# Performance work log

Measured on AMD Instinct MI355X. Metric: run time of the kernel, lower is better.

Reference implementation:

```python
import jax, jax.numpy as jnp
import numpy as np

VAR0, VAR1 = 0.1, 0.2   # cfg['variance']
THRESH = 0.5            # overlap_thresh
THETA = 0.01
NEGPOS = 3


def decode(loc, priors):
    # priors center-form [P,4]; returns point-form boxes [P,4]
    cxcy = priors[:, :2] + loc[:, :2] * VAR0 * priors[:, 2:]
    wh = priors[:, 2:] * jnp.exp(loc[:, 2:] * VAR1)
    return jnp.concatenate([cxcy - wh * 0.5, cxcy + wh * 0.5], axis=1)


def center_size(b):
    return jnp.concatenate([(b[:, :2] + b[:, 2:]) * 0.5, b[:, 2:] - b[:, :2]], axis=1)


def encode(matched, priors_c):
    # matched point-form [P,4], priors_c center-form [P,4]
    g_cxcy = ((matched[:, :2] + matched[:, 2:]) * 0.5 - priors_c[:, :2]) / (VAR0 * priors_c[:, 2:])
    g_wh = jnp.log((matched[:, 2:] - matched[:, :2]) / priors_c[:, 2:]) / VAR1
    return jnp.concatenate([g_cxcy, g_wh], axis=1)


def jaccard(a, b):
    # a [G,4], b [P,4] point form -> IoU [G,P]
    lt = jnp.maximum(a[:, None, :2], b[None, :, :2])
    rb = jnp.minimum(a[:, None, 2:], b[None, :, 2:])
    wh = jnp.clip(rb - lt, 0.0)
    inter = wh[..., 0] * wh[..., 1]
    area_a = ((a[:, 2] - a[:, 0]) * (a[:, 3] - a[:, 1]))[:, None]
    area_b = ((b[:, 2] - b[:, 0]) * (b[:, 3] - b[:, 1]))[None, :]
    return inter / (area_a + area_b - inter)


def _match_one(truths, labels, gt_mask, arm_loc, priors):
    # refine_match with arm_loc (use_ARM=True path)
    P = priors.shape[0]
    G = truths.shape[0]
    dec = decode(arm_loc, priors)                                 # [P,4]
    ov = jnp.where(gt_mask[:, None], jaccard(truths, dec), -1.0)  # [G,P], padded GT masked out
    best_prior_idx = jnp.argmax(ov, axis=1)                       # [G]
    best_truth_ov = jnp.max(ov, axis=0)                           # [P]
    best_truth_idx = jnp.argmax(ov, axis=0)                       # [P]
    safe = jnp.where(gt_mask, best_prior_idx, P)                  # OOB index -> dropped scatter
    best_truth_ov = best_truth_ov.at[safe].set(2.0, mode='drop')  # force-match each valid GT
    best_truth_idx = best_truth_idx.at[safe].set(jnp.arange(G), mode='drop')
    matched = truths[best_truth_idx]                              # [P,4]
    conf = jnp.where(best_truth_ov < THRESH, 0, labels[best_truth_idx])
    loc = encode(matched, center_size(dec))
    return loc, conf


def forward(arm_loc, arm_conf, odm_loc, odm_conf, priors, targets, num_gts):
    B, P, C = odm_conf.shape
    truths = targets[..., :4]
    labels = targets[..., 4].astype(jnp.int32)
    gt_mask = jnp.arange(targets.shape[1])[None, :] < num_gts[:, None]
    loc_t, conf_t = jax.vmap(_match_one, in_axes=(0, 0, 0, 0, None))(
        truths, labels, gt_mask,
        jax.lax.stop_gradient(arm_loc), jax.lax.stop_gradient(priors))
    loc_t = jax.lax.stop_gradient(loc_t)    # loc_t.requires_grad = False
    conf_t = jax.lax.stop_gradient(conf_t)

    # ARM objectness filter on positives
    p_obj = jax.nn.softmax(arm_conf, axis=2)[:, :, 1]
    pos = (conf_t > 0) & (p_obj > THETA)

    # masked smooth-L1 localization loss (sum)
    posf = pos[..., None].astype(odm_loc.dtype)
    d = jnp.abs(odm_loc * posf - loc_t * posf)
    loss_l = jnp.sum(jnp.where(d < 1.0, 0.5 * d * d, d - 0.5))

    # hard negative mining on per-prior softmax loss
    batch_conf = odm_conf.reshape(-1, C)
    lc = jax.nn.logsumexp(batch_conf, axis=1) - jnp.take_along_axis(
        batch_conf, conf_t.reshape(-1, 1), axis=1)[:, 0]
    lc = jnp.where(pos.reshape(-1), 0.0, lc).reshape(B, P)
    loss_idx = jnp.argsort(-lc, axis=1)
    idx_rank = jnp.argsort(loss_idx, axis=1)
    num_pos = jnp.sum(pos.astype(jnp.int32), axis=1, keepdims=True)  # [B,1]
    num_neg = jnp.minimum(NEGPOS * num_pos, P - 1)
    neg = idx_rank < num_neg
    mask = pos | neg

    # masked cross entropy (compute on zeroed-out logits like the original, then mask)
    conf_p = (odm_conf * mask[..., None].astype(odm_conf.dtype)).reshape(-1, C)
    tgt = jnp.where(mask, conf_t, 0).reshape(-1)
    logp = jax.nn.log_softmax(conf_p, axis=1)
    ce = -jnp.take_along_axis(logp, tgt[:, None], axis=1)[:, 0]
    loss_c = jnp.sum(ce * mask.reshape(-1).astype(ce.dtype))

    N = jnp.sum(num_pos).astype(jnp.float32)
    return loss_l / N, loss_c / N


def setup_inputs():
    key = jax.random.key(0)
    ks = jax.random.split(key, 10)
    B, P, C, G = 32, 16320, 21, 40
    arm_loc = jax.random.normal(ks[0], (B, P, 4), jnp.float32) * 0.1
    arm_conf = jax.random.normal(ks[1], (B, P, 2), jnp.float32)
    odm_loc = jax.random.normal(ks[2], (B, P, 4), jnp.float32) * 0.1
    odm_conf = jax.random.normal(ks[3], (B, P, C), jnp.float32)
    # priors in center form with positive sizes
    pc = jax.random.uniform(ks[4], (P, 2), jnp.float32, 0.1, 0.9)
    pwh = jax.random.uniform(ks[5], (P, 2), jnp.float32, 0.05, 0.3)
    priors = jnp.concatenate([pc, pwh], axis=1)
    # GT boxes in point form with positive area, labels in 1..C-1, padded to G=40
    gc = jax.random.uniform(ks[6], (B, G, 2), jnp.float32, 0.2, 0.8)
    gwh = jax.random.uniform(ks[7], (B, G, 2), jnp.float32, 0.05, 0.3)
    boxes = jnp.concatenate([gc - gwh * 0.5, gc + gwh * 0.5], axis=-1)
    labels = jax.random.randint(ks[8], (B, G, 1), 1, C).astype(jnp.float32)
    targets = jnp.concatenate([boxes, labels], axis=-1)
    num_gts = jax.random.randint(ks[9], (B,), 1, G + 1).astype(jnp.int32)
    return {"arm_loc": arm_loc, "arm_conf": arm_conf, "odm_loc": odm_loc,
            "odm_conf": odm_conf, "priors": priors, "targets": targets,
            "num_gts": num_gts}


def reference(arm_loc, arm_conf, odm_loc, odm_conf, priors, targets, num_gts):
    return forward(arm_loc, arm_conf, odm_loc, odm_conf, priors, targets, num_gts)
```

## Files before the change

kernel.cpp:

```cpp
#include <hip/hip_runtime.h>
#include <math.h>

#define VAR0 0.1f
#define VAR1 0.2f
#define THRESH 0.5f
#define THETA 0.01f
#define MAXG 64
#define BLK 256
#define SELT 1024
#define NCH 16
#define NB 4096
#define CAP 2048
#define NST 6

__device__ __forceinline__ float fdiv_fast(float a, float b) { return __fdividef(a, b); }

__device__ __forceinline__ float4 decode_box(float4 l, float4 pr) {
    float cx = pr.x + l.x * VAR0 * pr.z;
    float cy = pr.y + l.y * VAR0 * pr.w;
    float w = pr.z * __expf(l.z * VAR1);
    float h = pr.w * __expf(l.w * VAR1);
    return make_float4(cx - w * 0.5f, cy - h * 0.5f, cx + w * 0.5f, cy + h * 0.5f);
}

__device__ __forceinline__ float smooth_l1_sum(float4 ol, float4 t, float4 d) {
    float pcx = (d.x + d.z) * 0.5f, pcy = (d.y + d.w) * 0.5f;
    float pw = d.z - d.x, ph = d.w - d.y;
    float g0 = fdiv_fast((t.x + t.z) * 0.5f - pcx, VAR0 * pw);
    float g1 = fdiv_fast((t.y + t.w) * 0.5f - pcy, VAR0 * ph);
    float g2 = __logf(fdiv_fast(t.z - t.x, pw)) * (1.0f / VAR1);
    float g3 = __logf(fdiv_fast(t.w - t.y, ph)) * (1.0f / VAR1);
    float s = 0.f, dd;
    dd = fabsf(ol.x - g0); s += (dd < 1.f) ? 0.5f*dd*dd : dd - 0.5f;
    dd = fabsf(ol.y - g1); s += (dd < 1.f) ? 0.5f*dd*dd : dd - 0.5f;
    dd = fabsf(ol.z - g2); s += (dd < 1.f) ? 0.5f*dd*dd : dd - 0.5f;
    dd = fabsf(ol.w - g3); s += (dd < 1.f) ? 0.5f*dd*dd : dd - 0.5f;
    return s;
}

__device__ __forceinline__ float softmax_pobj(float2 c) {
    float mm = fmaxf(c.x, c.y);
    float e0 = __expf(c.x - mm), e1 = __expf(c.y - mm);
    return fdiv_fast(e1, e0 + e1);
}

__device__ __forceinline__ float iou_ov(float4 t, float areaA, float4 d, float areaB) {
    float lt0 = fmaxf(t.x, d.x), lt1 = fmaxf(t.y, d.y);
    float rb0 = fminf(t.z, d.z), rb1 = fminf(t.w, d.w);
    float w = rb0 - lt0; if (w < 0.f) w = 0.f;
    float h = rb1 - lt1; if (h < 0.f) h = 0.f;
    float inter = w * h;
    return fdiv_fast(inter, areaA + areaB - inter);
}

__device__ __forceinline__ unsigned wave_umax_bits(unsigned v) {
    int x = (int)v;
    int t;
    t = __builtin_amdgcn_update_dpp(0, x, 0x111, 0xf, 0xf, true);  x = (t > x) ? t : x;
    t = __builtin_amdgcn_update_dpp(0, x, 0x112, 0xf, 0xf, true);  x = (t > x) ? t : x;
    t = __builtin_amdgcn_update_dpp(0, x, 0x114, 0xf, 0xf, true);  x = (t > x) ? t : x;
    t = __builtin_amdgcn_update_dpp(0, x, 0x118, 0xf, 0xf, true);  x = (t > x) ? t : x;
    t = __builtin_amdgcn_update_dpp(0, x, 0x142, 0xa, 0xf, false); x = (t > x) ? t : x;
    t = __builtin_amdgcn_update_dpp(0, x, 0x143, 0xc, 0xf, false); x = (t > x) ? t : x;
    return (unsigned)__builtin_amdgcn_readlane(x, 63);
}

__global__ __launch_bounds__(BLK) void k_main2(
        const float* __restrict__ arm_loc, const float* __restrict__ priors,
        const float* __restrict__ arm_conf, const float* __restrict__ odm_loc,
        const float* __restrict__ odm_conf,
        const float* __restrict__ targets, const int* __restrict__ num_gts,
        float* __restrict__ ce, unsigned char* __restrict__ posm,
        unsigned* __restrict__ bb, unsigned long long* __restrict__ bpw,
        float* __restrict__ partL, int* __restrict__ partN, int* __restrict__ counter,
        int B, int P, int C, int G) {
    int b = blockIdx.y;
    int p0 = blockIdx.x * BLK;
    int tid = threadIdx.x;
    int p = p0 + tid;
    int lane = tid & 63, wid = tid >> 6;
    int wavebase = p0 + (tid & ~63);
    __shared__ float4 st4[MAXG];
    __shared__ float  stl[MAXG];
    __shared__ float  sarea[MAXG];
    __shared__ unsigned long long wk[4][MAXG];
    __shared__ float oc_s[BLK * 21];
    __shared__ float rl[BLK];
    __shared__ int   rc[BLK];
    __shared__ int sng;
    if (blockIdx.x == 0 && blockIdx.y == 0 && tid == 0) *counter = 0;
    if (tid == 0) sng = num_gts[b];
    for (int g = tid; g < G; g += BLK) {
        const float* tg = targets + (size_t)b * G * 5 + g * 5;
        float t0 = tg[0], t1 = tg[1], t2 = tg[2], t3 = tg[3];
        st4[g] = make_float4(t0, t1, t2, t3);
        stl[g] = tg[4];
        sarea[g] = (t2 - t0) * (t3 - t1);
    }
    __syncthreads();

    int nrows = P - p0; if (nrows > BLK) nrows = BLK;
    int nf = nrows * C;
    int nf4 = nf >> 2;
    const float4* ocb4 = (const float4*)(odm_conf + ((size_t)b * P + p0) * C);
    float4 stg[NST];
    #pragma unroll
    for (int r = 0; r < NST; ++r) {
        int idx = r * BLK + tid;
        stg[r] = (idx < nf4) ? ocb4[idx] : make_float4(0.f, 0.f, 0.f, 0.f);
    }

    int ng = sng;
    bool ok = p < P;
    float4 d = make_float4(0.f, 0.f, 0.f, 0.f);
    float areaB = 0.f;
    size_t i = (size_t)b * P + (ok ? p : 0);
    if (ok) {
        float4 l = ((const float4*)arm_loc)[i];
        float4 pr = ((const float4*)priors)[p];
        d = decode_box(l, pr);
        areaB = (d.z - d.x) * (d.w - d.y);
    }
    float bov = -2.0f; int bidx = 0;
    int g = 0;
    for (; g + 2 <= ng; g += 2) {
        float4 t0g = st4[g], t1g = st4[g + 1];
        unsigned vb0 = 0u, vb1 = 0u;
        if (ok) {
            float ov0 = iou_ov(t0g, sarea[g], d, areaB);
            float ov1 = iou_ov(t1g, sarea[g + 1], d, areaB);
            if (ov0 > bov) { bov = ov0; bidx = g; }
            if (ov1 > bov) { bov = ov1; bidx = g + 1; }
            vb0 = __float_as_uint(ov0);
            vb1 = __float_as_uint(ov1);
        }
        unsigned om0 = wave_umax_bits(vb0);
        unsigned om1 = wave_umax_bits(vb1);
        unsigned long long m0 = __ballot(ok && vb0 == om0);
        unsigned long long m1 = __ballot(ok && vb1 == om1);
        if (lane == 0) {
            unsigned long long k0 = 0ull, k1 = 0ull;
            if (m0) {
                int pw = wavebase + (int)__builtin_ctzll(m0);
                k0 = ((unsigned long long)om0 << 32)
                   | (unsigned long long)(0xFFFFFFFFu - (unsigned)pw);
            }
            if (m1) {
                int pw = wavebase + (int)__builtin_ctzll(m1);
                k1 = ((unsigned long long)om1 << 32)
                   | (unsigned long long)(0xFFFFFFFFu - (unsigned)pw);
            }
            wk[wid][g] = k0;
            wk[wid][g + 1] = k1;
        }
    }
    if (g < ng) {
        float4 tg = st4[g];
        unsigned vb = 0u;
        if (ok) {
            float ov = iou_ov(tg, sarea[g], d, areaB);
            if (ov > bov) { bov = ov; bidx = g; }
            vb = __float_as_uint(ov);
        }
        unsigned om = wave_umax_bits(vb);
        unsigned long long m = __ballot(ok && vb == om);
        if (lane == 0) {
            unsigned long long k0 = 0ull;
            if (m) {
                int pw = wavebase + (int)__builtin_ctzll(m);
                k0 = ((unsigned long long)om << 32)
                   | (unsigned long long)(0xFFFFFFFFu - (unsigned)pw);
            }
            wk[wid][g] = k0;
        }
    }

    float lsum = 0.f; int pc = 0;
    int conf_t = 0;
    if (ok) {
        conf_t = (bov < THRESH) ? 0 : (int)stl[bidx];
        float p_obj = softmax_pobj(((const float2*)arm_conf)[i]);
        bool pos = (conf_t > 0) && (p_obj > THETA);
        if (pos) {
            pc = 1;
            float4 ol = ((const float4*)odm_loc)[i];
            lsum = smooth_l1_sum(ol, st4[bidx], d);
        }
        posm[i] = pos ? 1 : 0;
        bb[i] = (__float_as_uint(bov) & 0xFFFFFFC0u) | (unsigned)bidx;
    }
    rl[tid] = lsum; rc[tid] = pc;

    #pragma unroll
    for (int r = 0; r < NST; ++r) {
        int idx = r * BLK + tid;
        if (idx < nf4) ((float4*)oc_s)[idx] = stg[r];
    }
    for (int t = (nf4 << 2) + tid; t < nf; t += BLK) oc_s[t] = ((const float*)ocb4)[t];
    __syncthreads();

    if (tid < ng) {
        unsigned long long k0 = wk[0][tid], k1 = wk[1][tid];
        unsigned long long k2 = wk[2][tid], k3 = wk[3][tid];
        unsigned long long m01 = k0 > k1 ? k0 : k1;
        unsigned long long m23 = k2 > k3 ? k2 : k3;
        unsigned long long m = m01 > m23 ? m01 : m23;
        bpw[(size_t)(b * G + tid) * gridDim.x + blockIdx.x] = m;
    }

    if (ok) {
        const float* oc = oc_s + tid * C;
        float mx = oc[0];
        for (int j = 1; j < C; ++j) mx = fmaxf(mx, oc[j]);
        float sume = 0.f;
        for (int j = 0; j < C; ++j) sume += __expf(oc[j] - mx);
        float lse = mx + __logf(sume);
        ce[i] = lse - oc[conf_t];
    }

    for (int off = BLK / 2; off > 0; off >>= 1) {
        if (tid < off) { rl[tid] += rl[tid + off]; rc[tid] += rc[tid + off]; }
        __syncthreads();
    }
    if (tid == 0) {
        partL[b * gridDim.x + blockIdx.x] = rl[0];
        partN[b * gridDim.x + blockIdx.x] = rc[0];
    }
}

__global__ __launch_bounds__(SELT) void k_tail(
        const float* __restrict__ arm_loc, const float* __restrict__ priors,
        const float* __restrict__ arm_conf, const float* __restrict__ odm_loc,
        const float* __restrict__ odm_conf,
        const float* __restrict__ targets, const int* __restrict__ num_gts,
        const unsigned long long* __restrict__ bpw, const unsigned* __restrict__ bb,
        float* __restrict__ ce, unsigned char* __restrict__ posm,
        const float* __restrict__ partL, const int* __restrict__ partN,
        float* __restrict__ partC, float* __restrict__ totL, int* __restrict__ npos,
        int* __restrict__ counter, float* __restrict__ out,
        int NBX, int B, int P, int C, int G) {
    int b = blockIdx.x;
    int tid = threadIdx.x;
    int lane = tid & 63, wid = tid >> 6;
    __shared__ int fp[MAXG];
    __shared__ float4 st4[MAXG];
    __shared__ float  stl[MAXG];
    __shared__ float  pdl[MAXG];
    __shared__ int    pdn[MAXG];
    __shared__ unsigned hist[NB];
    __shared__ float cv[CAP];
    __shared__ int   ci[CAP];
    __shared__ int   sums[SELT];
    __shared__ int   redi[16];
    __shared__ float redf[16];
    __shared__ int sh_base[16];
    __shared__ int sh_m, sh_b1, sh_k1, sh_npos, sh_istar, sh_kk, sh_cum, sh_last;
    __shared__ unsigned sh_T, sh_pref;
    __shared__ float sh_mx, sh_totl;
    __shared__ int sng;
    if (tid == 0) sng = num_gts[b];
    for (int g = tid; g < G; g += SELT) {
        const float* tg = targets + (size_t)b * G * 5 + g * 5;
        st4[g] = make_float4(tg[0], tg[1], tg[2], tg[3]);
        stl[g] = tg[4];
        pdl[g] = 0.f; pdn[g] = 0;
    }
    __syncthreads();
    int ng = sng;

    for (int g = wid; g < ng; g += 16) {
        const unsigned long long* src = bpw + (size_t)(b * G + g) * NBX;
        unsigned long long key = 0ull;
        for (int j = lane; j < NBX; j += 64) {
            unsigned long long v = src[j];
            if (v > key) key = v;
        }
        for (int off = 32; off > 0; off >>= 1) {
            unsigned long long o = __shfl_down(key, (unsigned)off, 64);
            if (o > key) key = o;
        }
        if (lane == 0) fp[g] = (int)(0xFFFFFFFFu - (unsigned)(key & 0xFFFFFFFFull));
    }
    __syncthreads();

    if (tid < ng) {
        int g = tid;
        bool dup = false;
        for (int g2 = g + 1; g2 < ng; ++g2) if (fp[g2] == fp[g]) { dup = true; break; }
        if (!dup) {
            int p = fp[g];
            size_t i = (size_t)b * P + p;
            unsigned bbv = bb[i];
            int old_bidx = (int)(bbv & 63u);
            bool old_ge = __uint_as_float(bbv & 0xFFFFFFC0u) >= THRESH;
            int old_ct = old_ge ? (int)stl[old_bidx] : 0;
            int new_ct = (int)stl[g];
            float p_obj = softmax_pobj(((const float2*)arm_conf)[i]);
            bool old_pos = (old_ct > 0) && (p_obj > THETA);
            bool new_pos = (p_obj > THETA);
            float dL = 0.f;
            if (old_pos || new_pos) {
                float4 l = ((const float4*)arm_loc)[i];
                float4 pr = ((const float4*)priors)[p];
                float4 d = decode_box(l, pr);
                float4 ol = ((const float4*)odm_loc)[i];
                if (old_pos) dL -= smooth_l1_sum(ol, st4[old_bidx], d);
                if (new_pos) dL += smooth_l1_sum(ol, st4[g], d);
            }
            pdl[g] = dL;
            pdn[g] = (new_pos ? 1 : 0) - (old_pos ? 1 : 0);
            const float* oc = odm_conf + i * (size_t)C;
            float ce_old = ce[i];
            float ce_new = (old_ct == new_ct) ? ce_old
                         : (ce_old + oc[old_ct] - oc[new_ct]);
            ce[i] = ce_new;
            posm[i] = new_pos ? 1 : 0;
        }
    }
    __syncthreads();

    int c0 = 0; float l0 = 0.f;
    for (int j = tid; j < NBX; j += SELT) { c0 += partN[b * NBX + j]; l0 += partL[b * NBX + j]; }
    for (int g = tid; g < G; g += SELT)   { c0 += pdn[g];             l0 += pdl[g]; }
    for (int off = 32; off > 0; off >>= 1) {
        c0 += __shfl_down(c0, (unsigned)off, 64);
        l0 += __shfl_down(l0, (unsigned)off, 64);
    }
    if (lane == 0) { redi[wid] = c0; redf[wid] = l0; }
    __syncthreads();
    if (tid < 64) {
        int v = (tid < 16) ? redi[tid] : 0;
        float f = (tid < 16) ? redf[tid] : 0.f;
        for (int off = 32; off > 0; off >>= 1) {
            v += __shfl_down(v, (unsigned)off, 64);
            f += __shfl_down(f, (unsigned)off, 64);
        }
        if (tid == 0) { sh_npos = v; sh_totl = f; }
    }
    __syncthreads();
    int npos_b = sh_npos;
    long K = 3L * npos_b;
    if (K > P - 1) K = P - 1;

    unsigned cb[NCH];
    unsigned lv[NCH];
    unsigned pmw = 0u;
    const unsigned* ceb = (const unsigned*)ce + (size_t)b * P;
    const unsigned char* pb = posm + (size_t)b * P;
    #pragma unroll
    for (int c = 0; c < NCH; ++c) {
        int i = c * SELT + tid;
        unsigned cbits = (i < P) ? ceb[i] : 0u;
        bool ps = (i < P) && (pb[i] != 0);
        cb[c] = cbits;
        if (ps) pmw |= (1u << c);
        lv[c] = ps ? 0u : cbits;
    }

    unsigned uT = 0xFFFFFFFFu; int istar = -1;
    if (K > 0) {
        float mx = 0.f;
        #pragma unroll
        for (int c = 0; c < NCH; ++c) mx = fmaxf(mx, __uint_as_float(lv[c]));
        for (int off = 32; off > 0; off >>= 1) mx = fmaxf(mx, __shfl_xor(mx, off, 64));
        if (lane == 0) redf[wid] = mx;
        __syncthreads();
        if (tid == 0) {
            float v = redf[0];
            for (int w = 1; w < 16; ++w) v = fmaxf(v, redf[w]);
            sh_mx = v;
        }
        __syncthreads();
        float vmax = sh_mx;
        float scale = (vmax > 0.f) ? ((float)NB / vmax) : 0.f;

        for (int j = tid; j < NB; j += SELT) hist[j] = 0u;
        __syncthreads();
        #pragma unroll
        for (int c = 0; c < NCH; ++c) {
            int i = c * SELT + tid;
            if (i < P) {
                int bn = (int)(__uint_as_float(lv[c]) * scale);
                if (bn > NB - 1) bn = NB - 1;
                atomicAdd(&hist[bn], 1u);
            }
        }
        __syncthreads();

        int s4 = (int)(hist[4*tid] + hist[4*tid+1] + hist[4*tid+2] + hist[4*tid+3]);
        sums[SELT - 1 - tid] = s4;
        __syncthreads();
        int x = sums[tid];
        int xs = x;
        for (int off = 1; off < 64; off <<= 1) {
            int o = __shfl_up(xs, (unsigned)off, 64);
            if (lane >= off) xs += o;
        }
        if (lane == 63) redi[wid] = xs;
        __syncthreads();
        if (tid < 64) {
            int v = (tid < 16) ? redi[tid] : 0;
            int vs = v;
            for (int off = 1; off < 16; off <<= 1) {
                int o = __shfl_up(vs, (unsigned)off, 64);
                if (lane >= off) vs += o;
            }
            if (tid < 16) redi[tid] = vs - v;
        }
        __syncthreads();
        int excl_rev = xs + redi[wid] - x;
        sums[tid] = excl_rev;
        __syncthreads();
        int suf = sums[SELT - 1 - tid];
        {
            int run = suf;
            for (int j = 3; j >= 0; --j) {
                int bin = 4 * tid + j;
                int h = (int)hist[bin];
                if ((long)run < K && K <= (long)run + h) { sh_b1 = bin; sh_k1 = (int)(K - run); }
                run += h;
            }
        }
        __syncthreads();
        int B1 = sh_b1, k1 = sh_k1;

        if (tid == 0) sh_m = 0;
        __syncthreads();
        #pragma unroll
        for (int c = 0; c < NCH; ++c) {
            int i = c * SELT + tid;
            if (i < P) {
                float f = __uint_as_float(lv[c]);
                int bn = (int)(f * scale);
                if (bn > NB - 1) bn = NB - 1;
                if (bn == B1) {
                    int pos = atomicAdd(&sh_m, 1);
                    if (pos < CAP) { cv[pos] = f; ci[pos] = i; }
                }
            }
        }
        __syncthreads();
        int m = sh_m;
        if (m <= CAP) {
            for (int j = tid; j < m; j += SELT) {
                float vj = cv[j]; int ij = ci[j]; int r = 0;
                for (int jj = 0; jj < m; ++jj) {
                    float vx = cv[jj];
                    r += (vx > vj || (vx == vj && ci[jj] < ij)) ? 1 : 0;
                }
                if (r == k1 - 1) { sh_T = __float_as_uint(vj); sh_istar = ij; }
            }
            __syncthreads();
            uT = sh_T; istar = sh_istar;
        } else {
            if (tid == 0) { sh_pref = 0u; sh_kk = (int)K; }
            __syncthreads();
            for (int bit = 30; bit >= 0; --bit) {
                unsigned pref = sh_pref;
                int kk = sh_kk;
                unsigned hi = pref >> (bit + 1);
                int cnt = 0;
                #pragma unroll
                for (int c = 0; c < NCH; ++c) {
                    int i = c * SELT + tid;
                    unsigned v = lv[c];
                    cnt += ((i < P) && ((v >> (bit + 1)) == hi) && ((v >> bit) & 1u)) ? 1 : 0;
                }
                for (int off = 32; off > 0; off >>= 1) cnt += __shfl_down(cnt, (unsigned)off, 64);
                if (lane == 0) redi[wid] = cnt;
                __syncthreads();
                if (tid < 64) {
                    int v = (tid < 16) ? redi[tid] : 0;
                    for (int off = 32; off > 0; off >>= 1) v += __shfl_down(v, (unsigned)off, 64);
                    if (tid == 0) {
                        if (kk <= v) sh_pref = pref | (1u << bit);
                        else sh_kk = kk - v;
                    }
                }
                __syncthreads();
            }
            unsigned T = sh_pref; int krem = sh_kk;
            if (tid == 0) { sh_istar = -1; sh_cum = 0; }
            __syncthreads();
            for (int c = 0; c < NCH; ++c) {
                int i = c * SELT + tid;
                bool eq = (i < P) && (lv[c] == T);
                unsigned long long mk = __ballot(eq);
                if (lane == 0) redi[wid] = (int)__popcll(mk);
                __syncthreads();
                if (tid < 64) {
                    int v = (tid < 16) ? redi[tid] : 0;
                    for (int off = 1; off < 16; off <<= 1) {
                        int o = __shfl_up(v, (unsigned)off, 64);
                        if (lane >= off) v += o;
                    }
                    if (tid < 16) sh_base[tid] = v;
                }
                __syncthreads();
                int cum = sh_cum;
                int base = (wid == 0) ? 0 : sh_base[wid - 1];
                if (eq) {
                    int r = cum + base + (int)__popcll(mk & ((1ull << lane) - 1ull));
                    if (r == krem - 1) sh_istar = i;
                }
                __syncthreads();
                if (tid == 0) sh_cum = cum + sh_base[15];
                __syncthreads();
                if (sh_cum >= krem) break;
            }
            __syncthreads();
            uT = T; istar = sh_istar;
        }
    }

    float cs = 0.f;
    #pragma unroll
    for (int c = 0; c < NCH; ++c) {
        int i = c * SELT + tid;
        if (i < P) {
            unsigned v = lv[c];
            bool sel = ((pmw >> c) & 1u) || (v > uT) || (v == uT && i <= istar);
            if (sel) cs += __uint_as_float(cb[c]);
        }
    }
    for (int off = 32; off > 0; off >>= 1) cs += __shfl_down(cs, (unsigned)off, 64);
    if (lane == 0) redf[wid] = cs;
    __syncthreads();
    if (tid < 64) {
        float v = (tid < 16) ? redf[tid] : 0.f;
        for (int off = 32; off > 0; off >>= 1) v += __shfl_down(v, (unsigned)off, 64);
        if (tid == 0) {
            partC[b] = v; npos[b] = npos_b; totL[b] = sh_totl;
            __threadfence();
            int old = atomicAdd(counter, 1);
            sh_last = (old == B - 1) ? 1 : 0;
        }
    }
    __syncthreads();

    if (sh_last && tid < 64) {
        float aL = 0.f, aC = 0.f; int aN = 0;
        if (tid < B) {
            aL = atomicAdd(&totL[tid], 0.0f);
            aC = atomicAdd(&partC[tid], 0.0f);
            aN = atomicAdd(&npos[tid], 0);
        }
        for (int off = 32; off > 0; off >>= 1) {
            aL += __shfl_down(aL, (unsigned)off, 64);
            aC += __shfl_down(aC, (unsigned)off, 64);
            aN += __shfl_down(aN, (unsigned)off, 64);
        }
        if (tid == 0) {
            float N = (float)aN;
            out[0] = aL / N;
            out[1] = aC / N;
        }
    }
}

extern "C" void kernel_launch(void* const* d_in, const int* in_sizes, int n_in,
                              void* d_out, int out_size, void* d_ws, size_t ws_size,
                              hipStream_t stream) {
    const float* arm_loc  = (const float*)d_in[0];
    const float* arm_conf = (const float*)d_in[1];
    const float* odm_loc  = (const float*)d_in[2];
    const float* odm_conf = (const float*)d_in[3];
    const float* priors   = (const float*)d_in[4];
    const float* targets  = (const float*)d_in[5];
    const int*   num_gts  = (const int*)d_in[6];
    float* out = (float*)d_out;

    int B = in_sizes[6];
    int P = in_sizes[4] / 4;
    int C = in_sizes[3] / (B * P);
    int G = in_sizes[5] / (B * 5);
    int NBX = (P + BLK - 1) / BLK;

    char* ws = (char*)d_ws;
    size_t off = 0;
    auto alloc = [&](size_t bytes) -> void* {
        void* ptr = ws + off;
        off = (off + bytes + 255) & ~(size_t)255;
        return ptr;
    };
    unsigned long long* bpw = (unsigned long long*)alloc((size_t)B * G * NBX * 8);
    unsigned* bb = (unsigned*)alloc((size_t)B * P * 4);
    float* ce  = (float*)alloc((size_t)B * P * sizeof(float));
    unsigned char* posm = (unsigned char*)alloc((size_t)B * P);
    float* partL = (float*)alloc((size_t)B * NBX * sizeof(float));
    int* partN   = (int*)alloc((size_t)B * NBX * sizeof(int));
    float* partC = (float*)alloc((size_t)B * sizeof(float));
    float* totL  = (float*)alloc((size_t)B * sizeof(float));
    int* npos    = (int*)alloc((size_t)B * sizeof(int));
    int* counter = (int*)alloc(sizeof(int));

    k_main2<<<dim3(NBX, B), BLK, 0, stream>>>(arm_loc, priors, arm_conf, odm_loc, odm_conf,
                                              targets, num_gts, ce, posm, bb, bpw,
                                              partL, partN, counter, B, P, C, G);
    k_tail<<<B, SELT, 0, stream>>>(arm_loc, priors, arm_conf, odm_loc, odm_conf,
                                   targets, num_gts, bpw, bb, ce, posm,
                                   partL, partN, partC, totL, npos, counter, out,
                                   NBX, B, P, C, G);
}
```

Before: 58.40 us.

## Pack positive flag into CE sign bit and recompute best-truth in tail

Removes the separate per-prior positive-mask and best-truth buffers. The positive flag is now stored in the sign bit of the cross-entropy value, and the tail kernel recomputes the old best-GT match for the few force-matched priors instead of reading it back. The softmax objectness test is replaced by an equivalent logit-difference comparison, which drops the exp and division. This cuts global writes and reads per prior at the cost of a small loop over GTs per forced prior in the tail. Clamping CE to non-negative keeps the sign-bit packing valid.

```diff
diff --git a/kernel.cpp b/kernel.cpp
--- a/kernel.cpp
+++ b/kernel.cpp
@@ -4,7 +4,7 @@
 #define VAR0 0.1f
 #define VAR1 0.2f
 #define THRESH 0.5f
-#define THETA 0.01f
+#define LTHETA -4.59511985f
 #define MAXG 64
 #define BLK 256
 #define SELT 1024
@@ -38,11 +38,7 @@
     return s;
 }
 
-__device__ __forceinline__ float softmax_pobj(float2 c) {
-    float mm = fmaxf(c.x, c.y);
-    float e0 = __expf(c.x - mm), e1 = __expf(c.y - mm);
-    return fdiv_fast(e1, e0 + e1);
-}
+__device__ __forceinline__ bool pos_logit(float2 c) { return (c.y - c.x) > LTHETA; }
 
 __device__ __forceinline__ float iou_ov(float4 t, float areaA, float4 d, float areaB) {
     float lt0 = fmaxf(t.x, d.x), lt1 = fmaxf(t.y, d.y);
@@ -70,8 +66,8 @@
         const float* __restrict__ arm_conf, const float* __restrict__ odm_loc,
         const float* __restrict__ odm_conf,
         const float* __restrict__ targets, const int* __restrict__ num_gts,
-        float* __restrict__ ce, unsigned char* __restrict__ posm,
-        unsigned* __restrict__ bb, unsigned long long* __restrict__ bpw,
+        float* __restrict__ ce,
+        unsigned long long* __restrict__ bpw,
         float* __restrict__ partL, int* __restrict__ partN, int* __restrict__ counter,
         int B, int P, int C, int G) {
     int b = blockIdx.y;
@@ -177,17 +173,16 @@
 
     float lsum = 0.f; int pc = 0;
     int conf_t = 0;
+    bool pos = false;
     if (ok) {
         conf_t = (bov < THRESH) ? 0 : (int)stl[bidx];
-        float p_obj = softmax_pobj(((const float2*)arm_conf)[i]);
-        bool pos = (conf_t > 0) && (p_obj > THETA);
+        float2 c = ((const float2*)arm_conf)[i];
+        pos = (conf_t > 0) && pos_logit(c);
         if (pos) {
             pc = 1;
             float4 ol = ((const float4*)odm_loc)[i];
             lsum = smooth_l1_sum(ol, st4[bidx], d);
         }
-        posm[i] = pos ? 1 : 0;
-        bb[i] = (__float_as_uint(bov) & 0xFFFFFFC0u) | (unsigned)bidx;
     }
     rl[tid] = lsum; rc[tid] = pc;
 
@@ -215,7 +210,8 @@
         float sume = 0.f;
         for (int j = 0; j < C; ++j) sume += __expf(oc[j] - mx);
         float lse = mx + __logf(sume);
-        ce[i] = lse - oc[conf_t];
+        float cev = lse - oc[conf_t];
+        ((unsigned*)ce)[i] = __float_as_uint(cev) | (pos ? 0x80000000u : 0u);
     }
 
     for (int off = BLK / 2; off > 0; off >>= 1) {
@@ -233,8 +229,8 @@
         const float* __restrict__ arm_conf, const float* __restrict__ odm_loc,
         const float* __restrict__ odm_conf,
         const float* __restrict__ targets, const int* __restrict__ num_gts,
-        const unsigned long long* __restrict__ bpw, const unsigned* __restrict__ bb,
-        float* __restrict__ ce, unsigned char* __restrict__ posm,
+        const unsigned long long* __restrict__ bpw,
+        float* __restrict__ ce,
         const float* __restrict__ partL, const int* __restrict__ partN,
         float* __restrict__ partC, float* __restrict__ totL, int* __restrict__ npos,
         int* __restrict__ counter, float* __restrict__ out,
@@ -290,19 +286,25 @@
         if (!dup) {
             int p = fp[g];
             size_t i = (size_t)b * P + p;
-            unsigned bbv = bb[i];
-            int old_bidx = (int)(bbv & 63u);
-            bool old_ge = __uint_as_float(bbv & 0xFFFFFFC0u) >= THRESH;
-            int old_ct = old_ge ? (int)stl[old_bidx] : 0;
+            float4 l = ((const float4*)arm_loc)[i];
+            float4 pr = ((const float4*)priors)[p];
+            float4 d = decode_box(l, pr);
+            float areaB = (d.z - d.x) * (d.w - d.y);
+            float bov = -2.0f; int old_bidx = 0;
+            for (int gg = 0; gg < ng; ++gg) {
+                float4 t = st4[gg];
+                float areaA = (t.z - t.x) * (t.w - t.y);
+                float ov = iou_ov(t, areaA, d, areaB);
+                if (ov > bov) { bov = ov; old_bidx = gg; }
+            }
+            int old_ct = (bov < THRESH) ? 0 : (int)stl[old_bidx];
             int new_ct = (int)stl[g];
-            float p_obj = softmax_pobj(((const float2*)arm_conf)[i]);
-            bool old_pos = (old_ct > 0) && (p_obj > THETA);
-            bool new_pos = (p_obj > THETA);
+            float2 c = ((const float2*)arm_conf)[i];
+            bool pl = pos_logit(c);
+            bool old_pos = (old_ct > 0) && pl;
+            bool new_pos = pl;
             float dL = 0.f;
             if (old_pos || new_pos) {
-                float4 l = ((const float4*)arm_loc)[i];
-                float4 pr = ((const float4*)priors)[p];
-                float4 d = decode_box(l, pr);
                 float4 ol = ((const float4*)odm_loc)[i];
                 if (old_pos) dL -= smooth_l1_sum(ol, st4[old_bidx], d);
                 if (new_pos) dL += smooth_l1_sum(ol, st4[g], d);
@@ -310,11 +312,10 @@
             pdl[g] = dL;
             pdn[g] = (new_pos ? 1 : 0) - (old_pos ? 1 : 0);
             const float* oc = odm_conf + i * (size_t)C;
-            float ce_old = ce[i];
+            float ce_old = fabsf(ce[i]);
             float ce_new = (old_ct == new_ct) ? ce_old
-                         : (ce_old + oc[old_ct] - oc[new_ct]);
-            ce[i] = ce_new;
-            posm[i] = new_pos ? 1 : 0;
+                         : fmaxf(ce_old + oc[old_ct] - oc[new_ct], 0.f);
+            ((unsigned*)ce)[i] = __float_as_uint(ce_new) | (new_pos ? 0x80000000u : 0u);
         }
     }
     __syncthreads();
@@ -346,15 +347,14 @@
     unsigned lv[NCH];
     unsigned pmw = 0u;
     const unsigned* ceb = (const unsigned*)ce + (size_t)b * P;
-    const unsigned char* pb = posm + (size_t)b * P;
     #pragma unroll
     for (int c = 0; c < NCH; ++c) {
         int i = c * SELT + tid;
-        unsigned cbits = (i < P) ? ceb[i] : 0u;
-        bool ps = (i < P) && (pb[i] != 0);
-        cb[c] = cbits;
+        unsigned sbits = (i < P) ? ceb[i] : 0u;
+        bool ps = (sbits >> 31) != 0u;
+        cb[c] = sbits & 0x7FFFFFFFu;
         if (ps) pmw |= (1u << c);
-        lv[c] = ps ? 0u : cbits;
+        lv[c] = ps ? 0u : sbits;
     }
 
     unsigned uT = 0xFFFFFFFFu; int istar = -1;
@@ -584,9 +584,7 @@
         return ptr;
     };
     unsigned long long* bpw = (unsigned long long*)alloc((size_t)B * G * NBX * 8);
-    unsigned* bb = (unsigned*)alloc((size_t)B * P * 4);
     float* ce  = (float*)alloc((size_t)B * P * sizeof(float));
-    unsigned char* posm = (unsigned char*)alloc((size_t)B * P);
     float* partL = (float*)alloc((size_t)B * NBX * sizeof(float));
     int* partN   = (int*)alloc((size_t)B * NBX * sizeof(int));
     float* partC = (float*)alloc((size_t)B * sizeof(float));
@@ -595,10 +593,10 @@
     int* counter = (int*)alloc(sizeof(int));
 
     k_main2<<<dim3(NBX, B), BLK, 0, stream>>>(arm_loc, priors, arm_conf, odm_loc, odm_conf,
-                                              targets, num_gts, ce, posm, bb, bpw,
+                                              targets, num_gts, ce, bpw,
                                               partL, partN, counter, B, P, C, G);
     k_tail<<<B, SELT, 0, stream>>>(arm_loc, priors, arm_conf, odm_loc, odm_conf,
-                                   targets, num_gts, bpw, bb, ce, posm,
+                                   targets, num_gts, bpw, ce,
                                    partL, partN, partC, totL, npos, counter, out,
                                    NBX, B, P, C, G);
 }
```

Result: no change. 57.52 us (-1.5%).
